# Kernel tuning notes

Hardware: AMD Instinct MI355X
Metric: run time of the kernel (lower is better)

Reference implementation:

```python
import jax, jax.numpy as jnp
import numpy as np

B, S, D, E, NH, R, L = 512, 23, 768, 8, 8, 256, 50
TOP_K = 2
LN_EPS = 1e-5  # torch LayerNorm default


def _ln(x, g, b):
    m = jnp.mean(x, axis=-1, keepdims=True)
    v = jnp.mean((x - m) ** 2, axis=-1, keepdims=True)
    return (x - m) * jax.lax.rsqrt(v + LN_EPS) * g + b


def setup_inputs() -> dict:
    key = jax.random.key(0)
    it = iter(jax.random.split(key, 32))
    def p(shape, scale=0.02):
        return jax.random.normal(next(it), shape, dtype=jnp.float32) * scale
    inp = {
        'section_embeddings': jax.random.normal(next(it), (B, S, D), dtype=jnp.float32),
        'existing': jax.random.randint(next(it), (B, S), 0, 2, dtype=jnp.int32),
        'missing_table': p((S, D), 0.05),
        # DeepPositionEncoder per expert (num_layers=3): D->R->R->R->D + LN(D)
        'dpe_w0': p((E, D, R)), 'dpe_b0': jnp.zeros((E, R), jnp.float32),
        'dpe_w1': p((E, R, R)), 'dpe_b1': jnp.zeros((E, R), jnp.float32),
        'dpe_w2': p((E, R, R)), 'dpe_b2': jnp.zeros((E, R), jnp.float32),
        'dpe_wo': p((E, R, D)), 'dpe_bo': jnp.zeros((E, D), jnp.float32),
        'dpe_ln_g': jnp.ones((E, D), jnp.float32), 'dpe_ln_b': jnp.zeros((E, D), jnp.float32),
        # fusion_mlp: cat([context,pos]) (2D)->R->D ; W1 split into context/pos halves
        'fus_w1c': p((E, D, R)), 'fus_w1p': p((E, D, R)), 'fus_b1': jnp.zeros((E, R), jnp.float32),
        'fus_w2': p((E, R, D)), 'fus_b2': jnp.zeros((E, D), jnp.float32),
        # gate_mlp: 2D->R->1, sigmoid
        'gate_w1c': p((E, D, R)), 'gate_w1p': p((E, D, R)), 'gate_b1': jnp.zeros((E, R), jnp.float32),
        'gate_w2': p((E, R, 1)), 'gate_b2': jnp.zeros((E, 1), jnp.float32),
        'exp_ln_g': jnp.ones((E, D), jnp.float32), 'exp_ln_b': jnp.zeros((E, D), jnp.float32),
        # router: 2D->R->E
        'rtr_w1': p((2 * D, R)), 'rtr_b1': jnp.zeros((R,), jnp.float32),
        'rtr_w2': p((R, E)), 'rtr_b2': jnp.zeros((E,), jnp.float32),
        # SectionDimReducer: D->D//2->R + LN(R)
        'red_w1': p((D, D // 2)), 'red_b1': jnp.zeros((D // 2,), jnp.float32),
        'red_w2': p((D // 2, R)), 'red_b2': jnp.zeros((R,), jnp.float32),
        'red_ln_g': jnp.ones((R,), jnp.float32), 'red_ln_b': jnp.zeros((R,), jnp.float32),
        # MultiheadAttention (embed_dim=R, heads=NH)
        'qkv_w': p((3, R, R)), 'qkv_b': jnp.zeros((3, R), jnp.float32),
        'out_w': p((R, R)), 'out_b': jnp.zeros((R,), jnp.float32),
        # predictor
        'pred_w': p((R, L)), 'pred_b': jnp.zeros((L,), jnp.float32),
    }
    return inp


def reference(section_embeddings, existing, missing_table,
              dpe_w0, dpe_b0, dpe_w1, dpe_b1, dpe_w2, dpe_b2, dpe_wo, dpe_bo,
              dpe_ln_g, dpe_ln_b,
              fus_w1c, fus_w1p, fus_b1, fus_w2, fus_b2,
              gate_w1c, gate_w1p, gate_b1, gate_w2, gate_b2,
              exp_ln_g, exp_ln_b,
              rtr_w1, rtr_b1, rtr_w2, rtr_b2,
              red_w1, red_b1, red_w2, red_b2, red_ln_g, red_ln_b,
              qkv_w, qkv_b, out_w, out_b, pred_w, pred_b):
    mask = existing.astype(section_embeddings.dtype)[..., None]         # [B,S,1]
    # masked mean context over present sections
    context = (section_embeddings * mask).sum(1) / (mask.sum(1) + 1e-8)  # [B,D]
    T = B * S
    default = jnp.broadcast_to(missing_table[None], (B, S, D)).reshape(T, D)
    ctx = jnp.broadcast_to(context[:, None, :], (B, S, D)).reshape(T, D)
    # --- all experts, dense (as in source) ---
    h = jax.nn.relu(jnp.einsum('td,edh->teh', default, dpe_w0) + dpe_b0)
    h = jax.nn.relu(jnp.einsum('teh,ehk->tek', h, dpe_w1) + dpe_b1)
    h = jax.nn.relu(jnp.einsum('teh,ehk->tek', h, dpe_w2) + dpe_b2)
    pos = _ln(jnp.einsum('teh,ehd->ted', h, dpe_wo) + dpe_bo + default[:, None, :],
              dpe_ln_g, dpe_ln_b)                                        # [T,E,D]
    hf = jax.nn.relu(jnp.einsum('td,edh->teh', ctx, fus_w1c)
                     + jnp.einsum('ted,edh->teh', pos, fus_w1p) + fus_b1)
    cand = jnp.einsum('teh,ehd->ted', hf, fus_w2) + fus_b2
    hg = jax.nn.relu(jnp.einsum('td,edh->teh', ctx, gate_w1c)
                     + jnp.einsum('ted,edh->teh', pos, gate_w1p) + gate_b1)
    gate = jax.nn.sigmoid(jnp.einsum('teh,eho->teo', hg, gate_w2) + gate_b2)  # [T,E,1]
    exp_out = _ln(gate * cand + (1.0 - gate) * ctx[:, None, :], exp_ln_g, exp_ln_b)  # [T,E,D]
    # --- router: softmax -> top-k -> sparse scatter ---
    rin = jnp.concatenate([default, ctx], axis=-1)                      # [T,2D]
    scores = jax.nn.relu(rin @ rtr_w1 + rtr_b1) @ rtr_w2 + rtr_b2       # [T,E]
    w = jax.nn.softmax(scores, axis=-1)
    tv, ti = jax.lax.top_k(w, TOP_K)
    sw = jnp.zeros_like(w).at[jnp.arange(T)[:, None], ti].set(tv)       # [T,E]
    imputed = jnp.einsum('ted,te->td', exp_out, sw).reshape(B, S, D)
    sec = mask * section_embeddings + (1.0 - mask) * imputed            # [B,S,D]
    # --- reducer ---
    x = jax.nn.gelu(sec @ red_w1 + red_b1, approximate=False)
    x = jax.nn.gelu(x @ red_w2 + red_b2, approximate=False)
    x = _ln(x, red_ln_g, red_ln_b)                                      # [B,S,R]
    # --- MHA self-attention over sections ---
    hd = R // NH
    q = (x @ qkv_w[0] + qkv_b[0]).reshape(B, S, NH, hd)
    k = (x @ qkv_w[1] + qkv_b[1]).reshape(B, S, NH, hd)
    v = (x @ qkv_w[2] + qkv_b[2]).reshape(B, S, NH, hd)
    att = jax.nn.softmax(jnp.einsum('bqhd,bkhd->bhqk', q, k) / np.sqrt(hd), axis=-1)
    o = jnp.einsum('bhqk,bkhd->bqhd', att, v).reshape(B, S, R)
    o = o @ out_w + out_b
    logits = o.mean(axis=1) @ pred_w + pred_b                           # [B,L]
    return logits
```

## Files before the change

### kernel.cpp

```cpp
#include <hip/hip_runtime.h>
#include <hip/hip_bf16.h>
#include <math.h>

#define BB  512
#define SS  23
#define DD  768
#define EE  8
#define NHH 8
#define RR  256
#define HDD 32
#define LL  50
#define HH2 384
#define TT  (BB*SS)
#define LN_EPS 1e-5f
#define MAXWORK 1536
#define NCTX 4352
#define NACAP 12288
#define CPAD 64

typedef short v8s __attribute__((ext_vector_type(8)));
typedef float v4f __attribute__((ext_vector_type(4)));

__device__ __forceinline__ float gelu(float v){
  return 0.5f*v*(1.f + erff(v*0.70710678118654752f));
}
__device__ __forceinline__ unsigned short f2b(float v){
  __hip_bfloat16 h = __float2bfloat16(v);
  return *reinterpret_cast<unsigned short*>(&h);
}

__device__ __forceinline__ float block_sum(float v, float* red, int nw){
  #pragma unroll
  for (int o = 32; o > 0; o >>= 1) v += __shfl_down(v, o, 64);
  int wid = threadIdx.x >> 6;
  __syncthreads();
  if ((threadIdx.x & 63) == 0) red[wid] = v;
  __syncthreads();
  float s = 0.f;
  for (int i = 0; i < nw; ++i) s += red[i];
  return s;
}

__global__ void k_context(const float* __restrict__ emb, const int* __restrict__ existing,
                          float* __restrict__ ctx, unsigned short* __restrict__ ctxbf){
  int b = blockIdx.x, tid = threadIdx.x;
  float acc0=0.f, acc1=0.f, acc2=0.f;
  int cnt = 0;
  for (int s = 0; s < SS; ++s){
    if (existing[b*SS + s]){
      ++cnt;
      const float* row = emb + ((size_t)(b*SS + s))*DD;
      acc0 += row[tid]; acc1 += row[tid+256]; acc2 += row[tid+512];
    }
  }
  float inv = 1.0f / ((float)cnt + 1e-8f);
  float v0 = acc0*inv, v1 = acc1*inv, v2 = acc2*inv;
  ctx[(size_t)b*DD + tid      ] = v0;
  ctx[(size_t)b*DD + tid + 256] = v1;
  ctx[(size_t)b*DD + tid + 512] = v2;
  ctxbf[(size_t)b*DD + tid      ] = f2b(v0);
  ctxbf[(size_t)b*DD + tid + 256] = f2b(v1);
  ctxbf[(size_t)b*DD + tid + 512] = f2b(v2);
}

__global__ void k_mtpad(const float* __restrict__ mt, unsigned short* __restrict__ mtbf){
  int row = blockIdx.x, tid = threadIdx.x;
  #pragma unroll
  for (int j = 0; j < 3; ++j){
    int d = tid + j*256;
    float v = (row < SS) ? mt[(size_t)row*DD + d] : 0.f;
    mtbf[(size_t)row*DD + d] = f2b(v);
  }
}

__global__ __launch_bounds__(256) void k_pack(
    const float* __restrict__ red_w1, const float* __restrict__ qkv_w,
    const float* __restrict__ out_w,  const float* __restrict__ fus_w1c,
    const float* __restrict__ gate_w1c, const float* __restrict__ fus_w2,
    const float* __restrict__ rtr_w1,
    const float* __restrict__ dpe_w0, const float* __restrict__ dpe_w1,
    const float* __restrict__ dpe_w2, const float* __restrict__ dpe_wo,
    const float* __restrict__ fus_w1p, const float* __restrict__ gate_w1p,
    const float* __restrict__ red_w2,
    unsigned short* __restrict__ Wr1t, unsigned short* __restrict__ Wqt,
    unsigned short* __restrict__ Wot,  unsigned short* __restrict__ Wct,
    unsigned short* __restrict__ Wf2t,
    unsigned short* __restrict__ W0t,  unsigned short* __restrict__ W1t,
    unsigned short* __restrict__ W2t,  unsigned short* __restrict__ Wot2,
    unsigned short* __restrict__ Wpgt, unsigned short* __restrict__ Wr1rt,
    unsigned short* __restrict__ Wr2t){
  int t = blockIdx.x, tid = threadIdx.x;
  const float* src; unsigned short* dst;
  int Nsrc, stride, tk, tn;
  if (t < 288){ src = red_w1; dst = Wr1t; Nsrc = 384; stride = 768; tk = t % 24; tn = t / 24; }
  else if (t < 480){
    int u = t - 288, m = u >> 6, v2 = u & 63;
    src = qkv_w + (size_t)m*256*256; dst = Wqt + (size_t)m*256*256;
    Nsrc = 256; stride = 256; tk = v2 & 7; tn = v2 >> 3;
  } else if (t < 544){
    int v2 = t - 480;
    src = out_w; dst = Wot; Nsrc = 256; stride = 256; tk = v2 & 7; tn = v2 >> 3;
  } else if (t < 2080){
    int u = t - 544, e = u / 192, v2 = u % 192;
    src = fus_w1c + (size_t)e*DD*RR; dst = Wct + (size_t)(e*256)*768;
    Nsrc = 256; stride = 768; tk = v2 % 24; tn = v2 / 24;
  } else if (t < 3616){
    int u = t - 2080, e = u / 192, v2 = u % 192;
    src = gate_w1c + (size_t)e*DD*RR; dst = Wct + (size_t)(2048 + e*256)*768;
    Nsrc = 256; stride = 768; tk = v2 % 24; tn = v2 / 24;
  } else if (t < 5152){
    int u = t - 3616, e = u / 192, v2 = u % 192;
    src = fus_w2 + (size_t)e*RR*DD; dst = Wf2t + (size_t)e*768*256;
    Nsrc = 768; stride = 256; tk = v2 & 7; tn = v2 >> 3;
  } else if (t < 5344){
    int u = t - 5152;
    src = rtr_w1 + (size_t)768*256; dst = Wct + (size_t)4096*768;
    Nsrc = 256; stride = 768; tk = u % 24; tn = u / 24;
  } else if (t < 6880){
    int u = t - 5344, e = u / 192, v2 = u % 192;
    src = dpe_w0 + (size_t)e*DD*RR; dst = W0t + (size_t)e*256*768;
    Nsrc = 256; stride = 768; tk = v2 % 24; tn = v2 / 24;
  } else if (t < 7392){
    int u = t - 6880, e = u / 64, v2 = u % 64;
    src = dpe_w1 + (size_t)e*RR*RR; dst = W1t + (size_t)e*256*256;
    Nsrc = 256; stride = 256; tk = v2 & 7; tn = v2 >> 3;
  } else if (t < 7904){
    int u = t - 7392, e = u / 64, v2 = u % 64;
    src = dpe_w2 + (size_t)e*RR*RR; dst = W2t + (size_t)e*256*256;
    Nsrc = 256; stride = 256; tk = v2 & 7; tn = v2 >> 3;
  } else if (t < 9440){
    int u = t - 7904, e = u / 192, v2 = u % 192;
    src = dpe_wo + (size_t)e*RR*DD; dst = Wot2 + (size_t)e*768*256;
    Nsrc = 768; stride = 256; tk = v2 & 7; tn = v2 >> 3;
  } else if (t < 10976){
    int u = t - 9440, e = u / 192, v2 = u % 192;
    src = fus_w1p + (size_t)e*DD*RR; dst = Wpgt + (size_t)e*512*768;
    Nsrc = 256; stride = 768; tk = v2 % 24; tn = v2 / 24;
  } else if (t < 12512){
    int u = t - 10976, e = u / 192, v2 = u % 192;
    src = gate_w1p + (size_t)e*DD*RR; dst = Wpgt + (size_t)e*512*768 + (size_t)256*768;
    Nsrc = 256; stride = 768; tk = v2 % 24; tn = v2 / 24;
  } else if (t < 12704){
    int u = t - 12512;
    src = rtr_w1; dst = Wr1rt;
    Nsrc = 256; stride = 768; tk = u % 24; tn = u / 24;
  } else {
    int u = t - 12704;
    src = red_w2; dst = Wr2t;
    Nsrc = 256; stride = 384; tk = u % 12; tn = u / 12;
  }
  __shared__ float lt[32][33];
  int i0 = tid >> 5, j = tid & 31;
  #pragma unroll
  for (int l = 0; l < 4; ++l){
    int i = i0 + l*8;
    lt[i][j] = src[(size_t)(tk*32 + i)*Nsrc + tn*32 + j];
  }
  __syncthreads();
  #pragma unroll
  for (int l = 0; l < 4; ++l){
    int i = i0 + l*8;
    dst[(size_t)(tn*32 + i)*stride + tk*32 + j] = f2b(lt[j][i]);
  }
}

__global__ __launch_bounds__(256) void k_gemm(
    const unsigned short* __restrict__ A, const unsigned short* __restrict__ Bt,
    const float* __restrict__ bias, float* __restrict__ C,
    int M, int N, int K, int epi){
  int m0 = blockIdx.x * 64, n0 = blockIdx.y * 64;
  int tid = threadIdx.x;
  int w = tid >> 6, lane = tid & 63;
  int fm = lane & 15, q = lane >> 4;
  __shared__ unsigned short As[64*72];
  __shared__ unsigned short Bs[64*72];
  v4f acc[4] = {};
  int sr = tid >> 2, scb = (tid & 3) * 16;
  const unsigned short* Aga = A + (size_t)(m0 + sr)*K + scb;
  const unsigned short* Bga = Bt + (size_t)(n0 + sr)*K + scb;
  unsigned short* Asd = As + sr*72 + scb;
  unsigned short* Bsd = Bs + sr*72 + scb;
  for (int k0 = 0; k0 < K; k0 += 64){
    uint4 a0 = *(const uint4*)(Aga + k0);
    uint4 a1 = *(const uint4*)(Aga + k0 + 8);
    uint4 b0 = *(const uint4*)(Bga + k0);
    uint4 b1 = *(const uint4*)(Bga + k0 + 8);
    __syncthreads();
    *(uint4*)Asd = a0; *(uint4*)(Asd + 8) = a1;
    *(uint4*)Bsd = b0; *(uint4*)(Bsd + 8) = b1;
    __syncthreads();
    const unsigned short* ap = As + (w*16 + fm)*72 + q*8;
    const unsigned short* bp = Bs + fm*72 + q*8;
    #pragma unroll
    for (int kk = 0; kk < 2; ++kk){
      v8s af = *(const v8s*)(ap + kk*32);
      #pragma unroll
      for (int j = 0; j < 4; ++j){
        v8s bf = *(const v8s*)(bp + j*16*72 + kk*32);
        acc[j] = __builtin_amdgcn_mfma_f32_16x16x32_bf16(af, bf, acc[j], 0, 0, 0);
      }
    }
  }
  #pragma unroll
  for (int j = 0; j < 4; ++j){
    int n = n0 + j*16 + fm;
    float bv = bias ? bias[n] : 0.f;
    if (epi == 3){
      unsigned short* Cp = (unsigned short*)C + (size_t)(m0 + w*16 + q*4)*N + n;
      #pragma unroll
      for (int r = 0; r < 4; ++r)
        Cp[(size_t)r*N] = f2b(gelu(acc[j][r] + bv));
    } else {
      float* Cp = C + (size_t)(m0 + w*16 + q*4)*N + n;
      #pragma unroll
      for (int r = 0; r < 4; ++r){
        float v = acc[j][r] + bv;
        if (epi == 2) v = gelu(v);
        Cp[(size_t)r*N] = v;
      }
    }
  }
}

__global__ __launch_bounds__(256) void k_gemmb(
    const unsigned short* __restrict__ A, size_t sA,
    const unsigned short* __restrict__ Bt, size_t sB,
    const float* __restrict__ bias, int sbias,
    void* __restrict__ C, size_t sC,
    int M, int N, int K, int epi){
  int e = blockIdx.z;
  const unsigned short* Ae = A + (size_t)e*sA;
  const unsigned short* Be = Bt + (size_t)e*sB;
  const float* biase = bias ? (bias + (size_t)e*sbias) : (const float*)nullptr;
  int m0 = blockIdx.x * 64, n0 = blockIdx.y * 64;
  int tid = threadIdx.x;
  int w = tid >> 6, lane = tid & 63;
  int fm = lane & 15, q = lane >> 4;
  __shared__ unsigned short As[64*72];
  __shared__ unsigned short Bs[64*72];
  v4f acc[4] = {};
  int sr = tid >> 2, scb = (tid & 3) * 16;
  const unsigned short* Aga = Ae + (size_t)(m0 + sr)*K + scb;
  const unsigned short* Bga = Be + (size_t)(n0 + sr)*K + scb;
  unsigned short* Asd = As + sr*72 + scb;
  unsigned short* Bsd = Bs + sr*72 + scb;
  for (int k0 = 0; k0 < K; k0 += 64){
    uint4 a0 = *(const uint4*)(Aga + k0);
    uint4 a1 = *(const uint4*)(Aga + k0 + 8);
    uint4 b0 = *(const uint4*)(Bga + k0);
    uint4 b1 = *(const uint4*)(Bga + k0 + 8);
    __syncthreads();
    *(uint4*)Asd = a0; *(uint4*)(Asd + 8) = a1;
    *(uint4*)Bsd = b0; *(uint4*)(Bsd + 8) = b1;
    __syncthreads();
    const unsigned short* ap = As + (w*16 + fm)*72 + q*8;
    const unsigned short* bp = Bs + fm*72 + q*8;
    #pragma unroll
    for (int kk = 0; kk < 2; ++kk){
      v8s af = *(const v8s*)(ap + kk*32);
      #pragma unroll
      for (int j = 0; j < 4; ++j){
        v8s bf = *(const v8s*)(bp + j*16*72 + kk*32);
        acc[j] = __builtin_amdgcn_mfma_f32_16x16x32_bf16(af, bf, acc[j], 0, 0, 0);
      }
    }
  }
  #pragma unroll
  for (int j = 0; j < 4; ++j){
    int n = n0 + j*16 + fm;
    float bv = biase ? biase[n] : 0.f;
    #pragma unroll
    for (int r = 0; r < 4; ++r){
      float v = acc[j][r] + bv;
      int m = m0 + w*16 + q*4 + r;
      if (epi == 0){
        unsigned short* Cb = (unsigned short*)C + (size_t)e*sC;
        Cb[(size_t)m*N + n] = f2b(fmaxf(v, 0.f));
      } else {
        float* Cf = (float*)C + (size_t)e*sC;
        Cf[(size_t)m*N + n] = v;
      }
    }
  }
}

__global__ void k_posLN(const float* __restrict__ dpeout, const float* __restrict__ mt,
                        const float* __restrict__ lng, const float* __restrict__ lnb,
                        unsigned short* __restrict__ posbf){
  int e = blockIdx.x >> 6, s = blockIdx.x & 63, tid = threadIdx.x;
  size_t ro = (size_t)(e*64 + s)*DD;
  if (s >= SS){
    for (int j = tid; j < DD; j += 256) posbf[ro + j] = 0;
    return;
  }
  __shared__ float red[8];
  float o[3];
  #pragma unroll
  for (int j = 0; j < 3; ++j){
    int d = tid + j*256;
    o[j] = dpeout[ro + d] + mt[(size_t)s*DD + d];
  }
  float mean = block_sum(o[0]+o[1]+o[2], red, 4) * (1.f/DD);
  float dv = 0.f;
  #pragma unroll
  for (int j = 0; j < 3; ++j){ float c = o[j]-mean; dv += c*c; }
  float rstd = rsqrtf(block_sum(dv, red, 4) * (1.f/DD) + LN_EPS);
  #pragma unroll
  for (int j = 0; j < 3; ++j){
    int d = tid + j*256;
    posbf[ro + d] = f2b((o[j]-mean)*rstd*lng[e*DD + d] + lnb[e*DD + d]);
  }
}

__global__ __launch_bounds__(256) void k_router(
    const float* __restrict__ emb, const int* __restrict__ existing,
    const float* __restrict__ rtrD, const float* __restrict__ ctxFGR,
    const float* __restrict__ rb1, const float* __restrict__ rw2,
    const float* __restrict__ rb2,
    int* __restrict__ cntE, int* __restrict__ listE,
    int* __restrict__ bp0, int* __restrict__ bp1, float* __restrict__ w01,
    unsigned short* __restrict__ secbf){
  int wv = threadIdx.x >> 6, lane = threadIdx.x & 63;
  int tid = threadIdx.x;
  int t = blockIdx.x*4 + wv;
  __shared__ int   easc[8];
  __shared__ int   slotA[8];
  int ex = existing[t];
  if (ex){
    const float4* src = (const float4*)(emb + (size_t)t*DD);
    uint2* dst = (uint2*)(secbf + (size_t)t*DD);
    #pragma unroll
    for (int j = 0; j < 3; ++j){
      float4 x = src[lane + j*64];
      uint2 pk;
      pk.x = (unsigned)f2b(x.x) | ((unsigned)f2b(x.y) << 16);
      pk.y = (unsigned)f2b(x.z) | ((unsigned)f2b(x.w) << 16);
      dst[lane + j*64] = pk;
    }
    if (lane == 0){ easc[2*wv] = -1; easc[2*wv+1] = -1; }
  } else {
    int b = t / SS, s = t - b*SS;
    const float* rtrC = ctxFGR + (size_t)b*NCTX + 4096;
    float acc[EE] = {};
    #pragma unroll
    for (int j = 0; j < 4; ++j){
      int idx = lane + j*64;
      float hr = fmaxf(rtrD[s*RR + idx] + rtrC[idx] + rb1[idx], 0.f);
      #pragma unroll
      for (int e = 0; e < EE; ++e) acc[e] += hr * rw2[idx*EE + e];
    }
    #pragma unroll
    for (int e = 0; e < EE; ++e)
      #pragma unroll
      for (int o = 32; o > 0; o >>= 1) acc[e] += __shfl_xor(acc[e], o, 64);
    if (lane == 0){
      float sc[EE];
      float m = -1e30f;
      #pragma unroll
      for (int e = 0; e < EE; ++e){ sc[e] = acc[e] + rb2[e]; m = fmaxf(m, sc[e]); }
      float w[EE]; float Z = 0.f;
      #pragma unroll
      for (int e = 0; e < EE; ++e){ w[e] = expf(sc[e]-m); Z += w[e]; }
      int i0 = 0;
      for (int e = 1; e < EE; ++e) if (w[e] > w[i0]) i0 = e;
      int i1 = -1;
      for (int e = 0; e < EE; ++e) if (e != i0 && (i1 < 0 || w[e] > w[i1])) i1 = e;
      float iz = 1.f/Z;
      easc[2*wv]   = i0; w01[2*t]   = w[i0]*iz;
      easc[2*wv+1] = i1; w01[2*t+1] = w[i1]*iz;
    }
  }
  __syncthreads();
  if (tid < EE){
    int e = tid, c = 0;
    #pragma unroll
    for (int j = 0; j < 8; ++j) if (easc[j] == e) ++c;
    if (c){
      int base = atomicAdd(&cntE[e*CPAD], c);
      int sl = base;
      #pragma unroll
      for (int j = 0; j < 8; ++j) if (easc[j] == e) slotA[j] = sl++;
    }
  }
  __syncthreads();
  if (tid < 8){
    int j = tid, e = easc[j];
    if (e >= 0){
      int tt = blockIdx.x*4 + (j >> 1);
      int sl = slotA[j];
      if (sl >= TT) sl = TT - 1;
      listE[e*TT + sl] = tt;
      int bp = (e << 16) | sl;
      if (j & 1) bp1[tt] = bp;
      else       bp0[tt] = bp;
    }
  }
}

__global__ void k_offsE(const int* __restrict__ cntE, int* __restrict__ offE,
                        int* __restrict__ workE, int* __restrict__ wtotE){
  if (threadIdx.x == 0){
    int acc = 0, wb = 0;
    for (int e = 0; e < EE; ++e){
      offE[e] = acc;
      int n = cntE[e*CPAD]; if (n > TT) n = TT;
      acc += n;
      int nb = (n + 63) >> 6;
      for (int j = 0; j < nb && wb < MAXWORK; ++j) workE[wb++] = (e << 16) | j;
    }
    wtotE[0] = wb;
  }
}

__global__ __launch_bounds__(256) void k_hfE(
    const float* __restrict__ ctxFGR, const float* __restrict__ posFG,
    const float* __restrict__ fb1,
    const float* __restrict__ gb1, const float* __restrict__ gw2,
    const float* __restrict__ gb2,
    const int* __restrict__ cntE, const int* __restrict__ offE,
    const int* __restrict__ listE,
    const int* __restrict__ workE, const int* __restrict__ wtotE,
    unsigned short* __restrict__ hfg, float* __restrict__ gatesg){
  int wi = blockIdx.x;
  if (wi >= wtotE[0]) return;
  int ent = workE[wi];
  int e = ent >> 16, chunk = ent & 0xffff;
  int n = cntE[e*CPAD]; if (n > TT) n = TT;
  int nt = n - chunk*64; if (nt > 64) nt = 64;
  int base = offE[e] + chunk*64;
  int tid = threadIdx.x, wv = tid >> 6, lane = tid & 63;
  __shared__ int tb[64], ts[64];
  if (tid < 64){
    int ok = tid < nt;
    int t = listE[e*TT + chunk*64 + (ok ? tid : 0)];
    tb[tid] = t/SS; ts[tid] = t - (t/SS)*SS;
  }
  __syncthreads();
  {
    int row = tid >> 2, cb = (tid & 3) * 64;
    if (row < nt){
      int b = tb[row], s = ts[row];
      const float4* cF = (const float4*)(ctxFGR + (size_t)b*NCTX + e*256 + cb);
      const float4* pF = (const float4*)(posFG + ((size_t)(e*64 + s))*512 + cb);
      const float4* bF = (const float4*)(fb1 + (size_t)e*RR + cb);
      uint2* dst = (uint2*)(hfg + (size_t)(base + row)*256 + cb);
      #pragma unroll
      for (int j = 0; j < 16; ++j){
        float4 a = cF[j], p = pF[j], bb = bF[j];
        uint2 pk;
        pk.x = (unsigned)f2b(fmaxf(a.x+p.x+bb.x, 0.f))
             | ((unsigned)f2b(fmaxf(a.y+p.y+bb.y, 0.f)) << 16);
        pk.y = (unsigned)f2b(fmaxf(a.z+p.z+bb.z, 0.f))
             | ((unsigned)f2b(fmaxf(a.w+p.w+bb.w, 0.f)) << 16);
        dst[j] = pk;
      }
    }
  }
  for (int ii = 0; ii < 16; ++ii){
    int row = wv*16 + ii;
    if (row < nt){
      int b = tb[row], s = ts[row];
      float g = 0.f;
      #pragma unroll
      for (int j = 0; j < 4; ++j){
        int idx = lane + j*64;
        float hg = fmaxf(ctxFGR[(size_t)b*NCTX + 2048 + e*256 + idx]
                         + posFG[((size_t)(e*64 + s))*512 + 256 + idx] + gb1[e*RR + idx], 0.f);
        g += hg * gw2[e*RR + idx];
      }
      #pragma unroll
      for (int o = 32; o > 0; o >>= 1) g += __shfl_xor(g, o, 64);
      if (lane == 0) gatesg[base + row] = 1.f/(1.f + expf(-(g + gb2[e])));
    }
  }
}

__global__ __launch_bounds__(256) void k_gemmE(
    const unsigned short* __restrict__ hfg, const unsigned short* __restrict__ Wf2t,
    const float* __restrict__ fb2, const float* __restrict__ ctx,
    const float* __restrict__ gatesg,
    const int* __restrict__ cntE, const int* __restrict__ offE,
    const int* __restrict__ listE,
    const int* __restrict__ workE, const int* __restrict__ wtotE,
    float* __restrict__ cand){
  int wi = blockIdx.x;
  if (wi >= wtotE[0]) return;
  int ent = workE[wi];
  int e = ent >> 16, chunk = ent & 0xffff;
  int n = cntE[e*CPAD]; if (n > TT) n = TT;
  int nt = n - chunk*64; if (nt > 64) nt = 64;
  int base = offE[e] + chunk*64;
  int nc = blockIdx.y;
  int tid = threadIdx.x, w = tid >> 6, lane = tid & 63;
  int fm = lane & 15, q = lane >> 4;
  __shared__ unsigned short As[64*72];
  __shared__ unsigned short Bs[64*72];
  __shared__ float gl[64];
  __shared__ int tbl[64];
  if (tid < 64){
    int ok = tid < nt;
    int t = listE[e*TT + chunk*64 + (ok ? tid : 0)];
    tbl[tid] = t/SS;
    gl[tid] = gatesg[base + (ok ? tid : 0)];
  }
  v4f acc[4] = {};
  int sr = tid >> 2, scb = (tid & 3) * 16;
  const unsigned short* Aga = hfg + (size_t)(base + sr)*256 + scb;
  const unsigned short* Bga = Wf2t + (size_t)e*768*256 + (size_t)(nc*64 + sr)*256 + scb;
  unsigned short* Asd = As + sr*72 + scb;
  unsigned short* Bsd = Bs + sr*72 + scb;
  for (int k0 = 0; k0 < 256; k0 += 64){
    uint4 a0 = *(const uint4*)(Aga + k0);
    uint4 a1 = *(const uint4*)(Aga + k0 + 8);
    uint4 b0 = *(const uint4*)(Bga + k0);
    uint4 b1 = *(const uint4*)(Bga + k0 + 8);
    __syncthreads();
    *(uint4*)Asd = a0; *(uint4*)(Asd + 8) = a1;
    *(uint4*)Bsd = b0; *(uint4*)(Bsd + 8) = b1;
    __syncthreads();
    const unsigned short* ap = As + (w*16 + fm)*72 + q*8;
    const unsigned short* bp = Bs + fm*72 + q*8;
    #pragma unroll
    for (int kk = 0; kk < 2; ++kk){
      v8s af = *(const v8s*)(ap + kk*32);
      #pragma unroll
      for (int j = 0; j < 4; ++j){
        v8s bf = *(const v8s*)(bp + j*16*72 + kk*32);
        acc[j] = __builtin_amdgcn_mfma_f32_16x16x32_bf16(af, bf, acc[j], 0, 0, 0);
      }
    }
  }
  #pragma unroll
  for (int j = 0; j < 4; ++j){
    int d = nc*64 + j*16 + fm;
    float fb2v = fb2[(size_t)e*DD + d];
    #pragma unroll
    for (int r = 0; r < 4; ++r){
      int row = w*16 + q*4 + r;
      if (row < nt){
        float g = gl[row];
        float cv = ctx[(size_t)tbl[row]*DD + d];
        cand[(size_t)(base + row)*DD + d] = g*(acc[j][r] + fb2v) + (1.f - g)*cv;
      }
    }
  }
}

__global__ void k_gather(const int* __restrict__ existing,
                         const int* __restrict__ bp0, const int* __restrict__ bp1,
                         const float* __restrict__ w01, const int* __restrict__ offE,
                         const float* __restrict__ cand,
                         const float* __restrict__ elng, const float* __restrict__ elnb,
                         unsigned short* __restrict__ secbf){
  int wv = threadIdx.x >> 6, lane = threadIdx.x & 63;
  int t = blockIdx.x*4 + wv;
  if (existing[t]) return;
  int b0v = bp0[t], b1v = bp1[t];
  int e0 = b0v >> 16, e1 = b1v >> 16;
  int g0 = offE[e0] + (b0v & 0xffff);
  int g1 = offE[e1] + (b1v & 0xffff);
  if (g0 >= NACAP) g0 = 0;
  if (g1 >= NACAP) g1 = 0;
  float w0 = w01[2*t], w1 = w01[2*t+1];
  float v0[12], v1[12];
  float s0 = 0.f, q0 = 0.f, s1 = 0.f, q1 = 0.f;
  #pragma unroll
  for (int j = 0; j < 12; ++j){
    int d = lane + j*64;
    v0[j] = cand[(size_t)g0*DD + d];
    v1[j] = cand[(size_t)g1*DD + d];
    s0 += v0[j]; q0 += v0[j]*v0[j];
    s1 += v1[j]; q1 += v1[j]*v1[j];
  }
  #pragma unroll
  for (int o = 32; o > 0; o >>= 1){
    s0 += __shfl_xor(s0, o, 64); q0 += __shfl_xor(q0, o, 64);
    s1 += __shfl_xor(s1, o, 64); q1 += __shfl_xor(q1, o, 64);
  }
  float mean0 = s0*(1.f/DD), mean1 = s1*(1.f/DD);
  float rstd0 = rsqrtf(q0*(1.f/DD) - mean0*mean0 + LN_EPS);
  float rstd1 = rsqrtf(q1*(1.f/DD) - mean1*mean1 + LN_EPS);
  #pragma unroll
  for (int j = 0; j < 12; ++j){
    int d = lane + j*64;
    float o0 = (v0[j]-mean0)*rstd0*elng[e0*DD + d] + elnb[e0*DD + d];
    float o1 = (v1[j]-mean1)*rstd1*elng[e1*DD + d] + elnb[e1*DD + d];
    secbf[(size_t)t*DD + d] = f2b(w0*o0 + w1*o1);
  }
}

__global__ void k_lnR(const float* __restrict__ x2f,
                      const float* __restrict__ lng, const float* __restrict__ lnb,
                      unsigned short* __restrict__ xrbf){
  int wv = threadIdx.x >> 6, lane = threadIdx.x & 63;
  int t = blockIdx.x*4 + wv;
  float v[4];
  float s = 0.f, q = 0.f;
  #pragma unroll
  for (int j = 0; j < 4; ++j){
    v[j] = x2f[(size_t)t*RR + lane + j*64];
    s += v[j]; q += v[j]*v[j];
  }
  #pragma unroll
  for (int o = 32; o > 0; o >>= 1){
    s += __shfl_xor(s, o, 64); q += __shfl_xor(q, o, 64);
  }
  float mean = s*(1.f/RR);
  float rstd = rsqrtf(q*(1.f/RR) - mean*mean + LN_EPS);
  #pragma unroll
  for (int j = 0; j < 4; ++j){
    int d = lane + j*64;
    xrbf[(size_t)t*RR + d] = f2b((v[j]-mean)*rstd*lng[d] + lnb[d]);
  }
}

__global__ void k_attn(const float* __restrict__ qcat, unsigned short* __restrict__ attnbf){
  int bh = blockIdx.x, b = bh / NHH, h = bh % NHH, tid = threadIdx.x;
  __shared__ float qs[SS][HDD], ks[SS][HDD], vs[SS][HDD];
  __shared__ float scr[SS][SS+1];
  for (int idx = tid; idx < SS*HDD; idx += 256){
    int s = idx / HDD, d = idx % HDD;
    size_t g = ((size_t)(b*SS + s))*768 + h*HDD + d;
    qs[s][d] = qcat[g]; ks[s][d] = qcat[g + 256]; vs[s][d] = qcat[g + 512];
  }
  __syncthreads();
  const float scale = 0.17677669529663687f;
  for (int idx = tid; idx < SS*SS; idx += 256){
    int qi = idx / SS, ki = idx % SS;
    float a = 0.f;
    #pragma unroll
    for (int d = 0; d < HDD; ++d) a += qs[qi][d]*ks[ki][d];
    scr[qi][ki] = a*scale;
  }
  __syncthreads();
  if (tid < SS){
    float m = -1e30f;
    for (int ki = 0; ki < SS; ++ki) m = fmaxf(m, scr[tid][ki]);
    float Z = 0.f;
    for (int ki = 0; ki < SS; ++ki){ float e2 = expf(scr[tid][ki]-m); scr[tid][ki] = e2; Z += e2; }
    float iz = 1.f/Z;
    for (int ki = 0; ki < SS; ++ki) scr[tid][ki] *= iz;
  }
  __syncthreads();
  for (int idx = tid; idx < SS*HDD; idx += 256){
    int qi = idx / HDD, d = idx % HDD;
    float a = 0.f;
    for (int ki = 0; ki < SS; ++ki) a += scr[qi][ki]*vs[ki][d];
    attnbf[((size_t)(b*SS + qi))*RR + h*HDD + d] = f2b(a);
  }
}

__global__ void k_final(const float* __restrict__ oproj, const float* __restrict__ pw,
                        const float* __restrict__ pb, float* __restrict__ out){
  int b = blockIdx.x, tid = threadIdx.x;
  __shared__ float om[RR];
  float a = 0.f;
  for (int s = 0; s < SS; ++s) a += oproj[((size_t)(b*SS + s))*RR + tid];
  om[tid] = a * (1.f/SS);
  __syncthreads();
  if (tid < LL){
    float acc = pb[tid];
    for (int h = 0; h < RR; ++h) acc += om[h]*pw[h*LL + tid];
    out[b*LL + tid] = acc;
  }
}

extern "C" void kernel_launch(void* const* d_in, const int* in_sizes, int n_in,
                              void* d_out, int out_size, void* d_ws, size_t ws_size,
                              hipStream_t stream){
  (void)in_sizes; (void)n_in; (void)out_size; (void)ws_size;
  const float* emb      = (const float*)d_in[0];
  const int*   existing = (const int*)d_in[1];
  const float* mt       = (const float*)d_in[2];
  const float* dpe_w0   = (const float*)d_in[3];
  const float* dpe_b0   = (const float*)d_in[4];
  const float* dpe_w1   = (const float*)d_in[5];
  const float* dpe_b1   = (const float*)d_in[6];
  const float* dpe_w2   = (const float*)d_in[7];
  const float* dpe_b2   = (const float*)d_in[8];
  const float* dpe_wo   = (const float*)d_in[9];
  const float* dpe_bo   = (const float*)d_in[10];
  const float* dpe_lng  = (const float*)d_in[11];
  const float* dpe_lnb  = (const float*)d_in[12];
  const float* fus_w1c  = (const float*)d_in[13];
  const float* fus_w1p  = (const float*)d_in[14];
  const float* fus_b1   = (const float*)d_in[15];
  const float* fus_w2   = (const float*)d_in[16];
  const float* fus_b2   = (const float*)d_in[17];
  const float* gate_w1c = (const float*)d_in[18];
  const float* gate_w1p = (const float*)d_in[19];
  const float* gate_b1  = (const float*)d_in[20];
  const float* gate_w2  = (const float*)d_in[21];
  const float* gate_b2  = (const float*)d_in[22];
  const float* exp_lng  = (const float*)d_in[23];
  const float* exp_lnb  = (const float*)d_in[24];
  const float* rtr_w1   = (const float*)d_in[25];
  const float* rtr_b1   = (const float*)d_in[26];
  const float* rtr_w2   = (const float*)d_in[27];
  const float* rtr_b2   = (const float*)d_in[28];
  const float* red_w1   = (const float*)d_in[29];
  const float* red_b1   = (const float*)d_in[30];
  const float* red_w2   = (const float*)d_in[31];
  const float* red_b2   = (const float*)d_in[32];
  const float* red_lng  = (const float*)d_in[33];
  const float* red_lnb  = (const float*)d_in[34];
  const float* qkv_w    = (const float*)d_in[35];
  const float* qkv_b    = (const float*)d_in[36];
  const float* out_w    = (const float*)d_in[37];
  const float* out_b    = (const float*)d_in[38];
  const float* pred_w   = (const float*)d_in[39];
  const float* pred_b   = (const float*)d_in[40];
  float* out = (float*)d_out;

  float* wsf = (float*)d_ws;
  size_t off = 0;
  float* ctx    = wsf + off; off += (size_t)BB*DD;
  unsigned short* ctxbf = (unsigned short*)(wsf + off); off += (size_t)BB*DD/2;
  float* ctxFGR = wsf + off; off += (size_t)BB*NCTX;
  int*   cntE   = (int*)(wsf + off); off += EE*CPAD;
  int*   workE  = (int*)(wsf + off); off += MAXWORK;
  int*   wtot   = (int*)(wsf + off); off += 64;
  int*   offE   = wtot + 8;
  float* regA   = wsf + off; off += (size_t)128*TT;
  int*   listE  = (int*)regA;
  int*   bp0    = (int*)regA + (size_t)EE*TT;
  int*   bp1    = (int*)regA + (size_t)(EE+1)*TT;
  float* w01    = regA + (size_t)(EE+2)*TT;
  unsigned short* attnbf = (unsigned short*)regA;
  float* regB   = wsf + off; off += (size_t)TT*DD/2;
  unsigned short* secbf = (unsigned short*)regB;
  float* oprojf = regB;
  float* regC   = wsf + off; off += (size_t)NACAP*DD;
  float* dpeout = regC;
  unsigned short* posbf = (unsigned short*)(regC + 393216);
  unsigned short* h0    = (unsigned short*)(regC + 589824);
  unsigned short* h1    = (unsigned short*)(regC + 655360);
  unsigned short* h2    = (unsigned short*)(regC + 720896);
  float* cand   = regC;
  unsigned short* x1bf = (unsigned short*)regC;
  float* x2f    = regC + 4718592;
  float* qcat   = regC;
  float* regD   = wsf + off; off += (size_t)NACAP*256/2;
  unsigned short* hfg  = (unsigned short*)regD;
  unsigned short* xrbf = (unsigned short*)regD;
  unsigned short* Wr1t = (unsigned short*)(wsf + off); off += (size_t)768*384/2;
  unsigned short* Wqt  = (unsigned short*)(wsf + off); off += (size_t)768*256/2;
  unsigned short* Wot  = (unsigned short*)(wsf + off); off += (size_t)256*256/2;
  unsigned short* Wct  = (unsigned short*)(wsf + off); off += (size_t)NCTX*768/2;
  unsigned short* Wf2t = (unsigned short*)(wsf + off); off += (size_t)EE*768*256/2;
  unsigned short* mtbf = (unsigned short*)(wsf + off); off += (size_t)64*768/2;
  unsigned short* W0t  = (unsigned short*)(wsf + off); off += (size_t)EE*256*768/2;
  unsigned short* W1t  = (unsigned short*)(wsf + off); off += (size_t)EE*256*256/2;
  unsigned short* W2t  = (unsigned short*)(wsf + off); off += (size_t)EE*256*256/2;
  unsigned short* Wot2 = (unsigned short*)(wsf + off); off += (size_t)EE*768*256/2;
  unsigned short* Wpgt = (unsigned short*)(wsf + off); off += (size_t)EE*512*768/2;
  unsigned short* Wr1rt= (unsigned short*)(wsf + off); off += (size_t)256*768/2;
  unsigned short* Wr2t = (unsigned short*)(wsf + off); off += (size_t)256*384/2;
  float* posFG  = wsf + off; off += (size_t)EE*64*512;
  float* rtrDp  = wsf + off; off += (size_t)64*256;
  float* gatesg = wsf + off; off += (size_t)NACAP;

  k_context<<<BB, 256, 0, stream>>>(emb, existing, ctx, ctxbf);
  k_mtpad  <<<64, 256, 0, stream>>>(mt, mtbf);
  k_pack   <<<12800, 256, 0, stream>>>(red_w1, qkv_w, out_w, fus_w1c, gate_w1c, fus_w2,
                                       rtr_w1, dpe_w0, dpe_w1, dpe_w2, dpe_wo,
                                       fus_w1p, gate_w1p, red_w2,
                                       Wr1t, Wqt, Wot, Wct, Wf2t,
                                       W0t, W1t, W2t, Wot2, Wpgt, Wr1rt, Wr2t);
  k_gemmb<<<dim3(1,4,8),  256, 0, stream>>>(mtbf, 0, W0t, (size_t)256*768,
                                            dpe_b0, 256, h0, (size_t)64*256,
                                            64, 256, 768, 0);
  k_gemmb<<<dim3(1,4,8),  256, 0, stream>>>(h0, (size_t)64*256, W1t, (size_t)256*256,
                                            dpe_b1, 256, h1, (size_t)64*256,
                                            64, 256, 256, 0);
  k_gemmb<<<dim3(1,4,8),  256, 0, stream>>>(h1, (size_t)64*256, W2t, (size_t)256*256,
                                            dpe_b2, 256, h2, (size_t)64*256,
                                            64, 256, 256, 0);
  k_gemmb<<<dim3(1,12,8), 256, 0, stream>>>(h2, (size_t)64*256, Wot2, (size_t)768*256,
                                            dpe_bo, 768, dpeout, (size_t)64*768,
                                            64, 768, 256, 1);
  k_posLN<<<512, 256, 0, stream>>>(dpeout, mt, dpe_lng, dpe_lnb, posbf);
  k_gemmb<<<dim3(1,8,8),  256, 0, stream>>>(posbf, (size_t)64*768, Wpgt, (size_t)512*768,
                                            (const float*)nullptr, 0, posFG, (size_t)64*512,
                                            64, 512, 768, 1);
  k_gemmb<<<dim3(1,4,1),  256, 0, stream>>>(mtbf, 0, Wr1rt, 0,
                                            (const float*)nullptr, 0, rtrDp, 0,
                                            64, 256, 768, 1);
  {
    dim3 g(BB/64, NCTX/64);
    k_gemm <<<g, 256, 0, stream>>>(ctxbf, Wct, (const float*)nullptr, ctxFGR,
                                   BB, NCTX, DD, 0);
  }
  hipMemsetAsync(cntE, 0, EE*CPAD*sizeof(int), stream);
  k_router <<<TT/4, 256, 0, stream>>>(emb, existing, rtrDp, ctxFGR, rtr_b1, rtr_w2, rtr_b2,
                                      cntE, listE, bp0, bp1, w01, secbf);
  k_offsE  <<<1, 64, 0, stream>>>(cntE, offE, workE, wtot);
  k_hfE    <<<384, 256, 0, stream>>>(ctxFGR, posFG, fus_b1,
                                     gate_b1, gate_w2, gate_b2,
                                     cntE, offE, listE, workE, wtot, hfg, gatesg);
  k_gemmE  <<<dim3(384,12), 256, 0, stream>>>(hfg, Wf2t, fus_b2, ctx, gatesg,
                                              cntE, offE, listE, workE, wtot, cand);
  k_gather <<<TT/4, 256, 0, stream>>>(existing, bp0, bp1, w01, offE, cand,
                                      exp_lng, exp_lnb, secbf);
  {
    dim3 g(TT/64, HH2/64);
    k_gemm <<<g, 256, 0, stream>>>(secbf, Wr1t, red_b1, (float*)x1bf, TT, HH2, DD, 3);
  }
  {
    dim3 g(TT/64, RR/64);
    k_gemm <<<g, 256, 0, stream>>>(x1bf, Wr2t, red_b2, x2f, TT, RR, HH2, 2);
  }
  k_lnR    <<<TT/4, 256, 0, stream>>>(x2f, red_lng, red_lnb, xrbf);
  {
    dim3 g(TT/64, 768/64);
    k_gemm <<<g, 256, 0, stream>>>(xrbf, Wqt, qkv_b, qcat, TT, 768, RR, 1);
  }
  k_attn   <<<BB*NHH, 256, 0, stream>>>(qcat, attnbf);
  {
    dim3 g(TT/64, RR/64);
    k_gemm <<<g, 256, 0, stream>>>(attnbf, Wot, out_b, oprojf, TT, RR, RR, 1);
  }
  k_final  <<<BB, 256, 0, stream>>>(oprojf, pred_w, pred_b, out);
}
```

Measured before the change: 464.6 us.

## Use 128x128 GEMM tiles, store expert candidates in bf16, fold small kernels

Replaces the 64x64 dense GEMM with a 128x128 tile version where each wave computes a 64x64 sub-tile, raising MFMA work per shared-memory load across all dense GEMMs. Expert candidate outputs are written and read as bf16 instead of fp32, halving that intermediate's traffic at some precision cost. The missing-table padding kernel and the cntE memset are folded into k_context, removing a launch and a memset. Larger tiles give fewer blocks (e.g. TT=11776 rows divides by 128 exactly), which may reduce occupancy on small GEMMs.

```diff
diff --git a/kernel.cpp b/kernel.cpp
--- a/kernel.cpp
+++ b/kernel.cpp
@@ -28,6 +28,10 @@
   __hip_bfloat16 h = __float2bfloat16(v);
   return *reinterpret_cast<unsigned short*>(&h);
 }
+__device__ __forceinline__ float b2f(unsigned short u){
+  unsigned int x = ((unsigned)u) << 16;
+  return __uint_as_float(x);
+}
 
 __device__ __forceinline__ float block_sum(float v, float* red, int nw){
   #pragma unroll
@@ -42,8 +46,19 @@
 }
 
 __global__ void k_context(const float* __restrict__ emb, const int* __restrict__ existing,
-                          float* __restrict__ ctx, unsigned short* __restrict__ ctxbf){
+                          const float* __restrict__ mt,
+                          float* __restrict__ ctx, unsigned short* __restrict__ ctxbf,
+                          unsigned short* __restrict__ mtbf, int* __restrict__ cntE){
   int b = blockIdx.x, tid = threadIdx.x;
+  if (b == 0 && tid < EE) cntE[tid*CPAD] = 0;
+  if (b < 64){
+    #pragma unroll
+    for (int j = 0; j < 3; ++j){
+      int d = tid + j*256;
+      float v = (b < SS) ? mt[(size_t)b*DD + d] : 0.f;
+      mtbf[(size_t)b*DD + d] = f2b(v);
+    }
+  }
   float acc0=0.f, acc1=0.f, acc2=0.f;
   int cnt = 0;
   for (int s = 0; s < SS; ++s){
@@ -61,16 +76,6 @@
   ctxbf[(size_t)b*DD + tid      ] = f2b(v0);
   ctxbf[(size_t)b*DD + tid + 256] = f2b(v1);
   ctxbf[(size_t)b*DD + tid + 512] = f2b(v2);
-}
-
-__global__ void k_mtpad(const float* __restrict__ mt, unsigned short* __restrict__ mtbf){
-  int row = blockIdx.x, tid = threadIdx.x;
-  #pragma unroll
-  for (int j = 0; j < 3; ++j){
-    int d = tid + j*256;
-    float v = (row < SS) ? mt[(size_t)row*DD + d] : 0.f;
-    mtbf[(size_t)row*DD + d] = f2b(v);
-  }
 }
 
 __global__ __launch_bounds__(256) void k_pack(
@@ -164,18 +169,19 @@
   }
 }
 
-__global__ __launch_bounds__(256) void k_gemm(
+__global__ __launch_bounds__(256) void k_gemm2(
     const unsigned short* __restrict__ A, const unsigned short* __restrict__ Bt,
     const float* __restrict__ bias, float* __restrict__ C,
     int M, int N, int K, int epi){
-  int m0 = blockIdx.x * 64, n0 = blockIdx.y * 64;
+  int m0 = blockIdx.x * 128, n0 = blockIdx.y * 128;
   int tid = threadIdx.x;
   int w = tid >> 6, lane = tid & 63;
+  int wr = w >> 1, wc = w & 1;
   int fm = lane & 15, q = lane >> 4;
-  __shared__ unsigned short As[64*72];
-  __shared__ unsigned short Bs[64*72];
-  v4f acc[4] = {};
-  int sr = tid >> 2, scb = (tid & 3) * 16;
+  __shared__ unsigned short As[128*72];
+  __shared__ unsigned short Bs[128*72];
+  v4f acc[4][4] = {};
+  int sr = tid >> 1, scb = (tid & 1) * 32;
   const unsigned short* Aga = A + (size_t)(m0 + sr)*K + scb;
   const unsigned short* Bga = Bt + (size_t)(n0 + sr)*K + scb;
   unsigned short* Asd = As + sr*72 + scb;
@@ -183,40 +189,56 @@
   for (int k0 = 0; k0 < K; k0 += 64){
     uint4 a0 = *(const uint4*)(Aga + k0);
     uint4 a1 = *(const uint4*)(Aga + k0 + 8);
+    uint4 a2 = *(const uint4*)(Aga + k0 + 16);
+    uint4 a3 = *(const uint4*)(Aga + k0 + 24);
     uint4 b0 = *(const uint4*)(Bga + k0);
     uint4 b1 = *(const uint4*)(Bga + k0 + 8);
+    uint4 b2 = *(const uint4*)(Bga + k0 + 16);
+    uint4 b3 = *(const uint4*)(Bga + k0 + 24);
     __syncthreads();
     *(uint4*)Asd = a0; *(uint4*)(Asd + 8) = a1;
+    *(uint4*)(Asd + 16) = a2; *(uint4*)(Asd + 24) = a3;
     *(uint4*)Bsd = b0; *(uint4*)(Bsd + 8) = b1;
+    *(uint4*)(Bsd + 16) = b2; *(uint4*)(Bsd + 24) = b3;
     __syncthreads();
-    const unsigned short* ap = As + (w*16 + fm)*72 + q*8;
-    const unsigned short* bp = Bs + fm*72 + q*8;
+    const unsigned short* ap = As + ((size_t)(wr*64 + fm))*72 + q*8;
+    const unsigned short* bp = Bs + ((size_t)(wc*64 + fm))*72 + q*8;
     #pragma unroll
     for (int kk = 0; kk < 2; ++kk){
-      v8s af = *(const v8s*)(ap + kk*32);
+      v8s af0 = *(const v8s*)(ap + 0*16*72 + kk*32);
+      v8s af1 = *(const v8s*)(ap + 1*16*72 + kk*32);
+      v8s af2 = *(const v8s*)(ap + 2*16*72 + kk*32);
+      v8s af3 = *(const v8s*)(ap + 3*16*72 + kk*32);
       #pragma unroll
       for (int j = 0; j < 4; ++j){
         v8s bf = *(const v8s*)(bp + j*16*72 + kk*32);
-        acc[j] = __builtin_amdgcn_mfma_f32_16x16x32_bf16(af, bf, acc[j], 0, 0, 0);
+        acc[0][j] = __builtin_amdgcn_mfma_f32_16x16x32_bf16(af0, bf, acc[0][j], 0, 0, 0);
+        acc[1][j] = __builtin_amdgcn_mfma_f32_16x16x32_bf16(af1, bf, acc[1][j], 0, 0, 0);
+        acc[2][j] = __builtin_amdgcn_mfma_f32_16x16x32_bf16(af2, bf, acc[2][j], 0, 0, 0);
+        acc[3][j] = __builtin_amdgcn_mfma_f32_16x16x32_bf16(af3, bf, acc[3][j], 0, 0, 0);
       }
     }
   }
   #pragma unroll
-  for (int j = 0; j < 4; ++j){
-    int n = n0 + j*16 + fm;
-    float bv = bias ? bias[n] : 0.f;
-    if (epi == 3){
-      unsigned short* Cp = (unsigned short*)C + (size_t)(m0 + w*16 + q*4)*N + n;
-      #pragma unroll
-      for (int r = 0; r < 4; ++r)
-        Cp[(size_t)r*N] = f2b(gelu(acc[j][r] + bv));
-    } else {
-      float* Cp = C + (size_t)(m0 + w*16 + q*4)*N + n;
-      #pragma unroll
-      for (int r = 0; r < 4; ++r){
-        float v = acc[j][r] + bv;
-        if (epi == 2) v = gelu(v);
-        Cp[(size_t)r*N] = v;
+  for (int i = 0; i < 4; ++i){
+    #pragma unroll
+    for (int j = 0; j < 4; ++j){
+      int n = n0 + wc*64 + j*16 + fm;
+      float bv = bias ? bias[n] : 0.f;
+      int mrow = m0 + wr*64 + i*16 + q*4;
+      if (epi == 3){
+        unsigned short* Cp = (unsigned short*)C + (size_t)mrow*N + n;
+        #pragma unroll
+        for (int r = 0; r < 4; ++r)
+          Cp[(size_t)r*N] = f2b(gelu(acc[i][j][r] + bv));
+      } else {
+        float* Cp = C + (size_t)mrow*N + n;
+        #pragma unroll
+        for (int r = 0; r < 4; ++r){
+          float v = acc[i][j][r] + bv;
+          if (epi == 2) v = gelu(v);
+          Cp[(size_t)r*N] = v;
+        }
       }
     }
   }
@@ -482,7 +504,7 @@
     const int* __restrict__ cntE, const int* __restrict__ offE,
     const int* __restrict__ listE,
     const int* __restrict__ workE, const int* __restrict__ wtotE,
-    float* __restrict__ cand){
+    unsigned short* __restrict__ candbf){
   int wi = blockIdx.x;
   if (wi >= wtotE[0]) return;
   int ent = workE[wi];
@@ -540,7 +562,7 @@
       if (row < nt){
         float g = gl[row];
         float cv = ctx[(size_t)tbl[row]*DD + d];
-        cand[(size_t)(base + row)*DD + d] = g*(acc[j][r] + fb2v) + (1.f - g)*cv;
+        candbf[(size_t)(base + row)*DD + d] = f2b(g*(acc[j][r] + fb2v) + (1.f - g)*cv);
       }
     }
   }
@@ -549,7 +571,7 @@
 __global__ void k_gather(const int* __restrict__ existing,
                          const int* __restrict__ bp0, const int* __restrict__ bp1,
                          const float* __restrict__ w01, const int* __restrict__ offE,
-                         const float* __restrict__ cand,
+                         const unsigned short* __restrict__ candbf,
                          const float* __restrict__ elng, const float* __restrict__ elnb,
                          unsigned short* __restrict__ secbf){
   int wv = threadIdx.x >> 6, lane = threadIdx.x & 63;
@@ -567,8 +589,8 @@
   #pragma unroll
   for (int j = 0; j < 12; ++j){
     int d = lane + j*64;
-    v0[j] = cand[(size_t)g0*DD + d];
-    v1[j] = cand[(size_t)g1*DD + d];
+    v0[j] = b2f(candbf[(size_t)g0*DD + d]);
+    v1[j] = b2f(candbf[(size_t)g1*DD + d]);
     s0 += v0[j]; q0 += v0[j]*v0[j];
     s1 += v1[j]; q1 += v1[j]*v1[j];
   }
@@ -736,7 +758,7 @@
   unsigned short* h0    = (unsigned short*)(regC + 589824);
   unsigned short* h1    = (unsigned short*)(regC + 655360);
   unsigned short* h2    = (unsigned short*)(regC + 720896);
-  float* cand   = regC;
+  unsigned short* candbf = (unsigned short*)regC;
   unsigned short* x1bf = (unsigned short*)regC;
   float* x2f    = regC + 4718592;
   float* qcat   = regC;
@@ -760,8 +782,7 @@
   float* rtrDp  = wsf + off; off += (size_t)64*256;
   float* gatesg = wsf + off; off += (size_t)NACAP;
 
-  k_context<<<BB, 256, 0, stream>>>(emb, existing, ctx, ctxbf);
-  k_mtpad  <<<64, 256, 0, stream>>>(mt, mtbf);
+  k_context<<<BB, 256, 0, stream>>>(emb, existing, mt, ctx, ctxbf, mtbf, cntE);
   k_pack   <<<12800, 256, 0, stream>>>(red_w1, qkv_w, out_w, fus_w1c, gate_w1c, fus_w2,
                                        rtr_w1, dpe_w0, dpe_w1, dpe_w2, dpe_wo,
                                        fus_w1p, gate_w1p, red_w2,
@@ -787,11 +808,10 @@
                                             (const float*)nullptr, 0, rtrDp, 0,
                                             64, 256, 768, 1);
   {
-    dim3 g(BB/64, NCTX/64);
-    k_gemm <<<g, 256, 0, stream>>>(ctxbf, Wct, (const float*)nullptr, ctxFGR,
-                                   BB, NCTX, DD, 0);
-  }
-  hipMemsetAsync(cntE, 0, EE*CPAD*sizeof(int), stream);
+    dim3 g(BB/128, NCTX/128);
+    k_gemm2 <<<g, 256, 0, stream>>>(ctxbf, Wct, (const float*)nullptr, ctxFGR,
+                                    BB, NCTX, DD, 0);
+  }
   k_router <<<TT/4, 256, 0, stream>>>(emb, existing, rtrDp, ctxFGR, rtr_b1, rtr_w2, rtr_b2,
                                       cntE, listE, bp0, bp1, w01, secbf);
   k_offsE  <<<1, 64, 0, stream>>>(cntE, offE, workE, wtot);
@@ -799,26 +819,26 @@
                                      gate_b1, gate_w2, gate_b2,
                                      cntE, offE, listE, workE, wtot, hfg, gatesg);
   k_gemmE  <<<dim3(384,12), 256, 0, stream>>>(hfg, Wf2t, fus_b2, ctx, gatesg,
-                                              cntE, offE, listE, workE, wtot, cand);
-  k_gather <<<TT/4, 256, 0, stream>>>(existing, bp0, bp1, w01, offE, cand,
+                                              cntE, offE, listE, workE, wtot, candbf);
+  k_gather <<<TT/4, 256, 0, stream>>>(existing, bp0, bp1, w01, offE, candbf,
                                       exp_lng, exp_lnb, secbf);
   {
-    dim3 g(TT/64, HH2/64);
-    k_gemm <<<g, 256, 0, stream>>>(secbf, Wr1t, red_b1, (float*)x1bf, TT, HH2, DD, 3);
+    dim3 g(TT/128, HH2/128);
+    k_gemm2 <<<g, 256, 0, stream>>>(secbf, Wr1t, red_b1, (float*)x1bf, TT, HH2, DD, 3);
   }
   {
-    dim3 g(TT/64, RR/64);
-    k_gemm <<<g, 256, 0, stream>>>(x1bf, Wr2t, red_b2, x2f, TT, RR, HH2, 2);
+    dim3 g(TT/128, RR/128);
+    k_gemm2 <<<g, 256, 0, stream>>>(x1bf, Wr2t, red_b2, x2f, TT, RR, HH2, 2);
   }
   k_lnR    <<<TT/4, 256, 0, stream>>>(x2f, red_lng, red_lnb, xrbf);
   {
-    dim3 g(TT/64, 768/64);
-    k_gemm <<<g, 256, 0, stream>>>(xrbf, Wqt, qkv_b, qcat, TT, 768, RR, 1);
+    dim3 g(TT/128, 768/128);
+    k_gemm2 <<<g, 256, 0, stream>>>(xrbf, Wqt, qkv_b, qcat, TT, 768, RR, 1);
   }
   k_attn   <<<BB*NHH, 256, 0, stream>>>(qcat, attnbf);
   {
-    dim3 g(TT/64, RR/64);
-    k_gemm <<<g, 256, 0, stream>>>(attnbf, Wot, out_b, oprojf, TT, RR, RR, 1);
+    dim3 g(TT/128, RR/128);
+    k_gemm2 <<<g, 256, 0, stream>>>(attnbf, Wot, out_b, oprojf, TT, RR, RR, 1);
   }
   k_final  <<<BB, 256, 0, stream>>>(oprojf, pred_w, pred_b, out);
 }
```

After: 499.5 us. +7.5%, slower.
